# Kernel optimization log

Hardware: AMD Instinct MI355X
Metric: run time of the kernel (lower is better)

## Reference

```python
import jax, jax.numpy as jnp
import numpy as np

N_HEADS = 16
GROUP_SIZE = 4
D_MODEL = 2048
N_GROUPS = N_HEADS // GROUP_SIZE  # 4 KV heads
HEAD_DIM = D_MODEL // N_HEADS     # 128
B, S = 2, 2048


def setup_inputs() -> dict:
    key = jax.random.key(0)
    ks = jax.random.split(key, 10)
    sd = 1.0 / np.sqrt(D_MODEL)
    inp = {
        "x": jax.random.normal(ks[0], (B, S, D_MODEL), dtype=jnp.float32),
        # per-position, per-pair rotation angles (llama-style freqs)
        "rotary_freqs": jax.random.uniform(ks[1], (S, HEAD_DIM // 2), dtype=jnp.float32) * 6.283,
        # weights stored as [in, out] so forward is x @ W + b
        "Wq": jax.random.normal(ks[2], (D_MODEL, D_MODEL), dtype=jnp.float32) * sd,
        "bq": jnp.zeros((D_MODEL,), dtype=jnp.float32),
        "Wk": jax.random.normal(ks[3], (D_MODEL, N_GROUPS * HEAD_DIM), dtype=jnp.float32) * sd,
        "bk": jnp.zeros((N_GROUPS * HEAD_DIM,), dtype=jnp.float32),
        "Wv": jax.random.normal(ks[4], (D_MODEL, N_GROUPS * HEAD_DIM), dtype=jnp.float32) * sd,
        "bv": jnp.zeros((N_GROUPS * HEAD_DIM,), dtype=jnp.float32),
        "Wo": jax.random.normal(ks[5], (D_MODEL, D_MODEL), dtype=jnp.float32) * sd,
        "bo": jnp.zeros((D_MODEL,), dtype=jnp.float32),
    }
    return inp


def _rope(t, cos, sin):
    # t: [B, S, H, head_dim]; cos/sin: [1, S, 1, head_dim//2]
    t2 = t.reshape(t.shape[:-1] + (HEAD_DIM // 2, 2))
    te, to = t2[..., 0], t2[..., 1]
    re = te * cos - to * sin
    ro = te * sin + to * cos
    return jnp.stack([re, ro], axis=-1).reshape(t.shape)


def reference(x, rotary_freqs, Wq, bq, Wk, bk, Wv, bv, Wo, bo):
    Bx, Sx, _ = x.shape
    q = (x @ Wq + bq).reshape(Bx, Sx, N_HEADS, HEAD_DIM)
    k = (x @ Wk + bk).reshape(Bx, Sx, N_GROUPS, HEAD_DIM)
    v = (x @ Wv + bv).reshape(Bx, Sx, N_GROUPS, HEAD_DIM)

    cos = jnp.cos(rotary_freqs)[None, :, None, :]
    sin = jnp.sin(rotary_freqs)[None, :, None, :]
    q = _rope(q, cos, sin)
    k = _rope(k, cos, sin)

    q = q.transpose(0, 2, 1, 3)  # [B, H, S, hd]
    k = k.transpose(0, 2, 1, 3)  # [B, G, S, hd]
    v = v.transpose(0, 2, 1, 3)  # [B, G, S, hd]

    rep = N_HEADS // N_GROUPS
    k = jnp.repeat(k, rep, axis=1)  # repeat_interleave over head dim
    v = jnp.repeat(v, rep, axis=1)

    scores = jnp.einsum("bhsd,bhtd->bhst", q, k) / jnp.sqrt(jnp.float32(HEAD_DIM))
    att = jax.nn.softmax(scores, axis=-1)
    out = jnp.einsum("bhst,bhtd->bhsd", att, v)  # [B, H, S, hd]
    out = out.transpose(0, 2, 1, 3).reshape(Bx, Sx, D_MODEL)
    return out @ Wo + bo
```

## Files before the change

kernel.cpp:

```cpp
#include <hip/hip_runtime.h>
#include <cstdint>
#include <cstddef>

#define NB 2
#define SEQ 2048
#define DMODEL 2048
#define NHEAD 16
#define HDIM 128
#define NGRP 4
#define NKV (NGRP * HDIM)
#define NQKV (DMODEL + 2 * NKV)
#define MROWS (NB * SEQ)
#define QSCALE_LOG2E 0.12751743f

typedef unsigned short u16_t;
typedef unsigned int u32_t;
typedef __bf16 bf16x8 __attribute__((ext_vector_type(8)));
typedef __bf16 bf16x4 __attribute__((ext_vector_type(4)));
typedef float f32x4 __attribute__((ext_vector_type(4)));

static __device__ __forceinline__ u16_t f2bf(float f) {
  u32_t u = __builtin_bit_cast(u32_t, f);
  u32_t r = u + 0x7FFFu + ((u >> 16) & 1u);
  return (u16_t)(r >> 16);
}


__global__ __launch_bounds__(256) void k_prep(
    const float* __restrict__ x, const float* __restrict__ rf,
    const float* __restrict__ bq, const float* __restrict__ bk, const float* __restrict__ bv,
    const float* __restrict__ Wq, const float* __restrict__ Wk,
    const float* __restrict__ Wv, const float* __restrict__ Wo,
    u16_t* __restrict__ xb, float* __restrict__ cosT, float* __restrict__ sinT,
    float* __restrict__ bqkv, u16_t* __restrict__ Wqkvt, u16_t* __restrict__ Wot) {
  __shared__ float tile[64][65];
  int bid = blockIdx.x, t = threadIdx.x;

  if (bid < 8192) {
    int i = bid * 256 + t;
    float4 v = ((const float4*)x)[i];
    uint2 pk;
    pk.x = (u32_t)f2bf(v.x) | ((u32_t)f2bf(v.y) << 16);
    pk.y = (u32_t)f2bf(v.z) | ((u32_t)f2bf(v.w) << 16);
    ((uint2*)xb)[i] = pk;
    return;
  }
  bid -= 8192;
  if (bid < 512) {
    int i = bid * 256 + t;
    float f = rf[i];
    cosT[i] = cosf(f);
    sinT[i] = sinf(f);
    return;
  }
  bid -= 512;
  if (bid < 12) {
    int i = bid * 256 + t;
    float v = (i < DMODEL) ? bq[i] : (i < DMODEL + NKV ? bk[i - DMODEL] : bv[i - DMODEL - NKV]);
    bqkv[i] = v;
    return;
  }
  bid -= 12;

  const float* W; u16_t* Wt; int N, n0, k0;
  if (bid < 1024) {
    W = Wq; Wt = Wqkvt; N = DMODEL;
    n0 = (bid & 31) * 64; k0 = (bid >> 5) * 64;
  } else if (bid < 1280) {
    int b2 = bid - 1024;
    W = Wk; Wt = Wqkvt + (size_t)DMODEL * DMODEL; N = NKV;
    n0 = (b2 & 7) * 64; k0 = (b2 >> 3) * 64;
  } else if (bid < 1536) {
    int b2 = bid - 1280;
    W = Wv; Wt = Wqkvt + (size_t)(DMODEL + NKV) * DMODEL; N = NKV;
    n0 = (b2 & 7) * 64; k0 = (b2 >> 3) * 64;
  } else {
    int b2 = bid - 1536;
    W = Wo; Wt = Wot; N = DMODEL;
    n0 = (b2 & 31) * 64; k0 = (b2 >> 5) * 64;
  }
  const int K = DMODEL;
#pragma unroll
  for (int pass = 0; pass < 4; ++pass) {
    int slot = pass * 256 + t;
    int r = slot >> 4, c4 = (slot & 15) * 4;
    float4 v = *(const float4*)(W + (size_t)(k0 + r) * N + n0 + c4);
    tile[r][c4] = v.x; tile[r][c4 + 1] = v.y; tile[r][c4 + 2] = v.z; tile[r][c4 + 3] = v.w;
  }
  __syncthreads();
  int nr = t >> 2, seg = t & 3;
  alignas(16) u16_t o[16];
#pragma unroll
  for (int kk = 0; kk < 16; ++kk) o[kk] = f2bf(tile[seg * 16 + kk][nr]);
  u16_t* dst = Wt + (size_t)(n0 + nr) * K + k0 + seg * 16;
  ((int4*)dst)[0] = ((const int4*)o)[0];
  ((int4*)dst)[1] = ((const int4*)o)[1];
}


template <int EPI>
__global__ __launch_bounds__(512, 4) void k_gemm(
    const u16_t* __restrict__ A, const u16_t* __restrict__ Bt, const float* __restrict__ bias,
    float* __restrict__ Cout, u16_t* __restrict__ Qb, u16_t* __restrict__ Kb,
    u16_t* __restrict__ Vt, const float* __restrict__ cosT, const float* __restrict__ sinT,
    int M, int N, int K) {
  __shared__ u16_t lds[32768];
  int tid = threadIdx.x;
  int wid = tid >> 6, lane = tid & 63;
  int l15 = lane & 15, l4 = lane >> 4;
  int wrow = wid >> 2, wcol = wid & 3;

  int m0 = blockIdx.y << 7, n0 = blockIdx.x << 7;

  f32x4 acc[4][2] = {};

  auto stage = [&](int t) {
    u16_t* Al = lds + (t & 1) * 8192;
    u16_t* Bl = lds + 16384 + (t & 1) * 8192;
    int kbase = t * 64;
#pragma unroll
    for (int ss = 0; ss < 2; ++ss) {
      int slot = tid + ss * 512;
      int row = slot >> 3, c = slot & 7;
      int cs = c ^ (row & 7);
      __builtin_amdgcn_global_load_lds(
          (const __attribute__((address_space(1))) u32_t*)(A + (size_t)(m0 + row) * K + kbase + cs * 8),
          (__attribute__((address_space(3))) u32_t*)(Al + slot * 8), 16, 0, 0);
      __builtin_amdgcn_global_load_lds(
          (const __attribute__((address_space(1))) u32_t*)(Bt + (size_t)(n0 + row) * K + kbase + cs * 8),
          (__attribute__((address_space(3))) u32_t*)(Bl + slot * 8), 16, 0, 0);
    }
  };

  stage(0);
  stage(1);

  const int NT = K >> 6;
  for (int t = 0; t < NT; ++t) {
    if (t == NT - 1) {
      asm volatile("s_waitcnt vmcnt(0)" ::: "memory");
    } else {
      asm volatile("s_waitcnt vmcnt(4)" ::: "memory");
    }
    __builtin_amdgcn_s_barrier();
    __builtin_amdgcn_sched_barrier(0);

    const u16_t* Acur = lds + (t & 1) * 8192;
    const u16_t* Bcur = lds + 16384 + (t & 1) * 8192;

#pragma unroll
    for (int kk = 0; kk < 2; ++kk) {
      int chunk = ((kk << 2) + l4) ^ (l15 & 7);
      bf16x8 af[4], bfr[2];
#pragma unroll
      for (int i = 0; i < 4; ++i)
        af[i] = *(const bf16x8*)(Acur + (wrow * 64 + i * 16 + l15) * 64 + chunk * 8);
#pragma unroll
      for (int j = 0; j < 2; ++j)
        bfr[j] = *(const bf16x8*)(Bcur + (wcol * 32 + j * 16 + l15) * 64 + chunk * 8);

      __builtin_amdgcn_s_setprio(1);
#pragma unroll
      for (int i = 0; i < 4; ++i)
#pragma unroll
        for (int j = 0; j < 2; ++j)
          acc[i][j] = __builtin_amdgcn_mfma_f32_16x16x32_bf16(af[i], bfr[j], acc[i][j], 0, 0, 0);
      __builtin_amdgcn_s_setprio(0);
    }

    __builtin_amdgcn_sched_barrier(0);
    __builtin_amdgcn_s_barrier();
    __builtin_amdgcn_sched_barrier(0);
    if (t + 2 < NT) stage(t + 2);
  }

  if (EPI == 0) {
#pragma unroll
    for (int j = 0; j < 2; ++j) {
      int n = n0 + wcol * 32 + j * 16 + l15;
      float bs = bias[n];
#pragma unroll
      for (int i = 0; i < 4; ++i) {
        int mbase = m0 + wrow * 64 + i * 16 + l4 * 4;
#pragma unroll
        for (int r = 0; r < 4; ++r)
          Cout[(size_t)(mbase + r) * N + n] = acc[i][j][r] + bs;
      }
    }
  } else {
    bool isV = (n0 >= DMODEL + NKV);
    bool isK = (n0 >= DMODEL) && !isV;
#pragma unroll
    for (int j = 0; j < 2; ++j) {
      int n = n0 + wcol * 32 + j * 16 + l15;
      float bs = bias[n];
      int d = n & (HDIM - 1);
      int p = d >> 1;
      bool evn = !(d & 1);
#pragma unroll
      for (int i = 0; i < 4; ++i) {
        int mbase = m0 + wrow * 64 + i * 16 + l4 * 4;
        if (isV) {
          int g = (n - DMODEL - NKV) >> 7;
          int b = mbase >> 11, s0 = mbase & (SEQ - 1);
          u16_t o[4];
#pragma unroll
          for (int r = 0; r < 4; ++r) o[r] = f2bf(acc[i][j][r] + bs);
          uint2 pk;
          pk.x = (u32_t)o[0] | ((u32_t)o[1] << 16);
          pk.y = (u32_t)o[2] | ((u32_t)o[3] << 16);
          *(uint2*)(Vt + ((size_t)(b * NGRP + g) * HDIM + d) * SEQ + s0) = pk;
        } else {
#pragma unroll
          for (int r = 0; r < 4; ++r) {
            int m = mbase + r;
            int b = m >> 11, s = m & (SEQ - 1);
            float val = acc[i][j][r] + bs;
            float pv = __shfl_xor(val, 1);
            float c = cosT[s * (HDIM / 2) + p];
            float sn = sinT[s * (HDIM / 2) + p];
            float outv = evn ? (val * c - pv * sn) : (pv * sn + val * c);
            if (isK) {
              int g = (n - DMODEL) >> 7;
              Kb[((size_t)(b * NGRP + g) * SEQ + s) * HDIM + d] = f2bf(outv);
            } else {
              int h = n >> 7;
              Qb[((size_t)(b * NHEAD + h) * SEQ + s) * HDIM + d] = f2bf(outv * QSCALE_LOG2E);
            }
          }
        }
      }
    }
  }
}


__global__ __launch_bounds__(256, 2) void k_attn(
    const u16_t* __restrict__ Qb, const u16_t* __restrict__ Kb, const u16_t* __restrict__ Vt,
    u16_t* __restrict__ attn_out) {
  __shared__ u16_t lds[40960];

  int tid = threadIdx.x, wid = tid >> 6, lane = tid & 63;
  int l15 = lane & 15, l4 = lane >> 4;
  int bh = blockIdx.y;
  int b = bh >> 4, h = bh & 15, g = h >> 2;
  int q0 = blockIdx.x * 128;
  const u16_t* Qhead = Qb + (size_t)(b * NHEAD + h) * SEQ * HDIM;
  const u16_t* Khead = Kb + (size_t)(b * NGRP + g) * SEQ * HDIM;
  const u16_t* Vhead = Vt + (size_t)(b * NGRP + g) * HDIM * SEQ;

  bf16x8 qfa[4], qfb[4];
#pragma unroll
  for (int kc = 0; kc < 4; ++kc) {
    qfa[kc] = *(const bf16x8*)(Qhead + (size_t)(q0 + wid * 32 + l15) * HDIM + kc * 32 + l4 * 8);
    qfb[kc] = *(const bf16x8*)(Qhead + (size_t)(q0 + wid * 32 + 16 + l15) * HDIM + kc * 32 + l4 * 8);
  }

  f32x4 oa[8] = {}, ob[8] = {};
  f32x4 lav = {0.f, 0.f, 0.f, 0.f}, lbv = {0.f, 0.f, 0.f, 0.f};

  auto stageK = [&](int kv0, int ks) {
    u16_t* Kl = lds + ks * 8192;
#pragma unroll
    for (int ss = 0; ss < 4; ++ss) {
      int slot = tid + ss * 256;
      int rK = slot >> 4;
      int cK = (slot & 15) ^ ((rK & 3) | (((rK >> 3) & 1) << 2));
      __builtin_amdgcn_global_load_lds(
          (const __attribute__((address_space(1))) u32_t*)(Khead + (size_t)(kv0 + rK) * HDIM + cK * 8),
          (__attribute__((address_space(3))) u32_t*)(Kl + slot * 8), 16, 0, 0);
    }
  };
  auto stageV = [&](int kv0, int vs) {
    u16_t* Vl = lds + 24576 + vs * 8192;
#pragma unroll
    for (int ss = 0; ss < 4; ++ss) {
      int slot = tid + ss * 256;
      int rV = slot >> 3, cV = (slot & 7) ^ (rV & 7);
      __builtin_amdgcn_global_load_lds(
          (const __attribute__((address_space(1))) u32_t*)(Vhead + (size_t)rV * SEQ + kv0 + cV * 8),
          (__attribute__((address_space(3))) u32_t*)(Vl + slot * 8), 16, 0, 0);
    }
  };

  auto qk = [&](int ks, f32x4 (&Sa)[4], f32x4 (&Sb)[4]) {
    const u16_t* Kcur = lds + ks * 8192;
#pragma unroll
    for (int kc = 0; kc < 4; ++kc) {
#pragma unroll
      for (int kvb = 0; kvb < 4; ++kvb) {
        int row = (l15 >> 2) * 8 + ((kvb & 1) << 2) + (l15 & 3) + ((kvb >> 1) << 5);
        int chunk = ((kc << 2) + l4) ^ (l15 & 7);
        bf16x8 kf = *(const bf16x8*)(Kcur + row * 128 + chunk * 8);
        Sa[kvb] = __builtin_amdgcn_mfma_f32_16x16x32_bf16(kf, qfa[kc], Sa[kvb], 0, 0, 0);
        Sb[kvb] = __builtin_amdgcn_mfma_f32_16x16x32_bf16(kf, qfb[kc], Sb[kvb], 0, 0, 0);
      }
    }
  };

  auto expand = [&](f32x4 (&Sa)[4], f32x4 (&Sb)[4], bf16x8 (&pfa)[2], bf16x8 (&pfb)[2]) {
    bf16x4 pa[4], pb[4];
#pragma unroll
    for (int kvb = 0; kvb < 4; ++kvb) {
#pragma unroll
      for (int r = 0; r < 4; ++r) {
        float ea = __builtin_amdgcn_exp2f(Sa[kvb][r]);
        float eb = __builtin_amdgcn_exp2f(Sb[kvb][r]);
        lav[r] += ea; lbv[r] += eb;
        pa[kvb][r] = (__bf16)ea;
        pb[kvb][r] = (__bf16)eb;
      }
    }
#pragma unroll
    for (int kc2 = 0; kc2 < 2; ++kc2) {
      uint2 alo = __builtin_bit_cast(uint2, pa[kc2 * 2]);
      uint2 ahi = __builtin_bit_cast(uint2, pa[kc2 * 2 + 1]);
      uint4 wa; wa.x = alo.x; wa.y = alo.y; wa.z = ahi.x; wa.w = ahi.y;
      pfa[kc2] = __builtin_bit_cast(bf16x8, wa);
      uint2 blo = __builtin_bit_cast(uint2, pb[kc2 * 2]);
      uint2 bhi = __builtin_bit_cast(uint2, pb[kc2 * 2 + 1]);
      uint4 wb; wb.x = blo.x; wb.y = blo.y; wb.z = bhi.x; wb.w = bhi.y;
      pfb[kc2] = __builtin_bit_cast(bf16x8, wb);
    }
  };

  auto pv = [&](int vs, bf16x8 (&pfa)[2], bf16x8 (&pfb)[2]) {
    const u16_t* Vcur = lds + 24576 + vs * 8192;
#pragma unroll
    for (int kc2 = 0; kc2 < 2; ++kc2) {
#pragma unroll
      for (int dcb = 0; dcb < 8; ++dcb) {
        int chunk = ((kc2 << 2) + l4) ^ (l15 & 7);
        bf16x8 vf = *(const bf16x8*)(Vcur + (dcb * 16 + l15) * 64 + chunk * 8);
        oa[dcb] = __builtin_amdgcn_mfma_f32_16x16x32_bf16(vf, pfa[kc2], oa[dcb], 0, 0, 0);
        ob[dcb] = __builtin_amdgcn_mfma_f32_16x16x32_bf16(vf, pfb[kc2], ob[dcb], 0, 0, 0);
      }
    }
  };

  const int NT = SEQ / 64;

  auto step = [&](int t, bool last, f32x4 (&Ia)[4], f32x4 (&Ib)[4],
                  f32x4 (&Oa)[4], f32x4 (&Ob)[4]) {
    bf16x8 pfa[2], pfb[2];
    expand(Ia, Ib, pfa, pfb);
    if (last) {
      asm volatile("s_waitcnt vmcnt(4)" ::: "memory");
    } else {
      asm volatile("s_waitcnt vmcnt(8)" ::: "memory");
    }
    __builtin_amdgcn_s_barrier();
    __builtin_amdgcn_sched_barrier(0);
#pragma unroll
    for (int z = 0; z < 4; ++z)
#pragma unroll
      for (int r = 0; r < 4; ++r) { Oa[z][r] = 0.f; Ob[z][r] = 0.f; }
    __builtin_amdgcn_s_setprio(1);
    pv(t & 1, pfa, pfb);
    qk((t + 1) % 3, Oa, Ob);
    __builtin_amdgcn_s_setprio(0);
    __builtin_amdgcn_sched_barrier(0);
    __builtin_amdgcn_s_barrier();
    __builtin_amdgcn_sched_barrier(0);
    if (t + 3 < NT) stageK((t + 3) * 64, t % 3);
    if (t + 2 < NT) stageV((t + 2) * 64, t & 1);
  };

  f32x4 sA[4] = {}, sB[4] = {}, tA[4], tB[4];

  stageK(0, 0);
  stageK(64, 1);
  stageV(0, 0);
  asm volatile("s_waitcnt vmcnt(8)" ::: "memory");
  __builtin_amdgcn_s_barrier();
  __builtin_amdgcn_sched_barrier(0);
  stageK(128, 2);
  stageV(64, 1);
  qk(0, sA, sB);

  for (int p = 0; p < 15; ++p) {
    step(2 * p, false, sA, sB, tA, tB);
    step(2 * p + 1, false, tA, tB, sA, sB);
  }
  step(30, true, sA, sB, tA, tB);
  {
    bf16x8 pfa[2], pfb[2];
    expand(tA, tB, pfa, pfb);
    asm volatile("s_waitcnt vmcnt(0)" ::: "memory");
    __builtin_amdgcn_s_barrier();
    __builtin_amdgcn_sched_barrier(0);
    pv(1, pfa, pfb);
  }

  float la = lav[0] + lav[1] + lav[2] + lav[3];
  float lb = lbv[0] + lbv[1] + lbv[2] + lbv[3];
  la += __shfl_xor(la, 16); la += __shfl_xor(la, 32);
  lb += __shfl_xor(lb, 16); lb += __shfl_xor(lb, 32);
  float inva = 1.0f / la, invb = 1.0f / lb;

#pragma unroll
  for (int half = 0; half < 2; ++half) {
    u16_t* Owave = lds + half * 8704 + wid * 2176;
    const f32x4* oacc = half ? ob : oa;
    float inv = half ? invb : inva;
#pragma unroll
    for (int dcb = 0; dcb < 8; ++dcb) {
      bf16x4 ov;
#pragma unroll
      for (int r = 0; r < 4; ++r) ov[r] = (__bf16)(oacc[dcb][r] * inv);
      *(uint2*)(Owave + l15 * 136 + dcb * 16 + l4 * 4) = __builtin_bit_cast(uint2, ov);
    }
#pragma unroll
    for (int pass = 0; pass < 4; ++pass) {
      int rowq = pass * 4 + l4;
      int4 v = *(const int4*)(Owave + rowq * 136 + l15 * 8);
      int s = q0 + wid * 32 + half * 16 + rowq;
      *(int4*)(attn_out + ((size_t)(b * SEQ + s)) * DMODEL + h * HDIM + l15 * 8) = v;
    }
  }
}


extern "C" void kernel_launch(void* const* d_in, const int* in_sizes, int n_in,
                              void* d_out, int out_size, void* d_ws, size_t ws_size,
                              hipStream_t stream) {
  (void)in_sizes; (void)n_in; (void)out_size; (void)ws_size;
  const float* x  = (const float*)d_in[0];
  const float* rf = (const float*)d_in[1];
  const float* Wq = (const float*)d_in[2];
  const float* bq = (const float*)d_in[3];
  const float* Wk = (const float*)d_in[4];
  const float* bk = (const float*)d_in[5];
  const float* Wv = (const float*)d_in[6];
  const float* bv = (const float*)d_in[7];
  const float* Wo = (const float*)d_in[8];
  const float* bo = (const float*)d_in[9];
  float* out = (float*)d_out;

  char* ws = (char*)d_ws;
  u16_t* xb    = (u16_t*)ws;  ws += (size_t)MROWS * DMODEL * 2;
  u16_t* Wqkvt = (u16_t*)ws;  ws += (size_t)NQKV * DMODEL * 2;
  u16_t* Wot   = (u16_t*)ws;  ws += (size_t)DMODEL * DMODEL * 2;
  float* bqkv  = (float*)ws;  ws += (size_t)NQKV * 4;
  float* cosT  = (float*)ws;  ws += (size_t)SEQ * (HDIM / 2) * 4;
  float* sinT  = (float*)ws;  ws += (size_t)SEQ * (HDIM / 2) * 4;
  u16_t* Qb    = (u16_t*)ws;  ws += (size_t)NB * NHEAD * SEQ * HDIM * 2;
  u16_t* Kb    = (u16_t*)ws;  ws += (size_t)NB * NGRP * SEQ * HDIM * 2;
  u16_t* Vt    = (u16_t*)ws;  ws += (size_t)NB * NGRP * HDIM * SEQ * 2;
  u16_t* attn  = xb;

  k_prep<<<11276, 256, 0, stream>>>(x, rf, bq, bk, bv, Wq, Wk, Wv, Wo,
                                    xb, cosT, sinT, bqkv, Wqkvt, Wot);

  k_gemm<1><<<dim3(NQKV / 128, MROWS / 128), 512, 0, stream>>>(
      xb, Wqkvt, bqkv, nullptr, Qb, Kb, Vt, cosT, sinT, MROWS, NQKV, DMODEL);

  dim3 ga(SEQ / 128, NB * NHEAD);
  k_attn<<<ga, 256, 0, stream>>>(Qb, Kb, Vt, attn);

  k_gemm<0><<<dim3(DMODEL / 128, MROWS / 128), 512, 0, stream>>>(
      attn, Wot, bo, out, nullptr, nullptr, nullptr, nullptr, nullptr, MROWS, DMODEL, DMODEL);
}
```

Measured before the change: 177.3 us.

## Double-buffer K and V together in attention and shrink LDS footprint

Replaces the triple-buffered K plus double-buffered V staging with one combined double-buffered K/V stage, cutting shared memory from 80 KB to 64 KB per block. Each step now waits for all outstanding loads (vmcnt(0)) instead of leaving the next tile in flight, which simplifies the pipeline and removes the special-case last step. The softmax row-sum accumulator also collapses from a 4-wide vector to a scalar. The shallower prefetch exposes more global-load latency, and the scalar sum adds a serial dependency chain in the exp loop.

```diff
diff --git a/kernel.cpp b/kernel.cpp
--- a/kernel.cpp
+++ b/kernel.cpp
@@ -238,7 +238,7 @@
 __global__ __launch_bounds__(256, 2) void k_attn(
     const u16_t* __restrict__ Qb, const u16_t* __restrict__ Kb, const u16_t* __restrict__ Vt,
     u16_t* __restrict__ attn_out) {
-  __shared__ u16_t lds[40960];
+  __shared__ u16_t lds[32768];
 
   int tid = threadIdx.x, wid = tid >> 6, lane = tid & 63;
   int l15 = lane & 15, l4 = lane >> 4;
@@ -257,10 +257,11 @@
   }
 
   f32x4 oa[8] = {}, ob[8] = {};
-  f32x4 lav = {0.f, 0.f, 0.f, 0.f}, lbv = {0.f, 0.f, 0.f, 0.f};
-
-  auto stageK = [&](int kv0, int ks) {
-    u16_t* Kl = lds + ks * 8192;
+  float la = 0.f, lb = 0.f;
+
+  auto stage = [&](int kv0, int bufIdx) {
+    u16_t* Kl = lds + bufIdx * 8192;
+    u16_t* Vl = lds + 16384 + bufIdx * 8192;
 #pragma unroll
     for (int ss = 0; ss < 4; ++ss) {
       int slot = tid + ss * 256;
@@ -269,13 +270,6 @@
       __builtin_amdgcn_global_load_lds(
           (const __attribute__((address_space(1))) u32_t*)(Khead + (size_t)(kv0 + rK) * HDIM + cK * 8),
           (__attribute__((address_space(3))) u32_t*)(Kl + slot * 8), 16, 0, 0);
-    }
-  };
-  auto stageV = [&](int kv0, int vs) {
-    u16_t* Vl = lds + 24576 + vs * 8192;
-#pragma unroll
-    for (int ss = 0; ss < 4; ++ss) {
-      int slot = tid + ss * 256;
       int rV = slot >> 3, cV = (slot & 7) ^ (rV & 7);
       __builtin_amdgcn_global_load_lds(
           (const __attribute__((address_space(1))) u32_t*)(Vhead + (size_t)rV * SEQ + kv0 + cV * 8),
@@ -283,8 +277,8 @@
     }
   };
 
-  auto qk = [&](int ks, f32x4 (&Sa)[4], f32x4 (&Sb)[4]) {
-    const u16_t* Kcur = lds + ks * 8192;
+  auto qk = [&](int bufIdx, f32x4 (&Sa)[4], f32x4 (&Sb)[4]) {
+    const u16_t* Kcur = lds + bufIdx * 8192;
 #pragma unroll
     for (int kc = 0; kc < 4; ++kc) {
 #pragma unroll
@@ -306,7 +300,7 @@
       for (int r = 0; r < 4; ++r) {
         float ea = __builtin_amdgcn_exp2f(Sa[kvb][r]);
         float eb = __builtin_amdgcn_exp2f(Sb[kvb][r]);
-        lav[r] += ea; lbv[r] += eb;
+        la += ea; lb += eb;
         pa[kvb][r] = (__bf16)ea;
         pb[kvb][r] = (__bf16)eb;
       }
@@ -324,8 +318,8 @@
     }
   };
 
-  auto pv = [&](int vs, bf16x8 (&pfa)[2], bf16x8 (&pfb)[2]) {
-    const u16_t* Vcur = lds + 24576 + vs * 8192;
+  auto pv = [&](int bufIdx, bf16x8 (&pfa)[2], bf16x8 (&pfb)[2]) {
+    const u16_t* Vcur = lds + 16384 + bufIdx * 8192;
 #pragma unroll
     for (int kc2 = 0; kc2 < 2; ++kc2) {
 #pragma unroll
@@ -338,17 +332,10 @@
     }
   };
 
-  const int NT = SEQ / 64;
-
-  auto step = [&](int t, bool last, f32x4 (&Ia)[4], f32x4 (&Ib)[4],
-                  f32x4 (&Oa)[4], f32x4 (&Ob)[4]) {
+  auto step = [&](int t, f32x4 (&Ia)[4], f32x4 (&Ib)[4], f32x4 (&Oa)[4], f32x4 (&Ob)[4]) {
     bf16x8 pfa[2], pfb[2];
     expand(Ia, Ib, pfa, pfb);
-    if (last) {
-      asm volatile("s_waitcnt vmcnt(4)" ::: "memory");
-    } else {
-      asm volatile("s_waitcnt vmcnt(8)" ::: "memory");
-    }
+    asm volatile("s_waitcnt vmcnt(0)" ::: "memory");
     __builtin_amdgcn_s_barrier();
     __builtin_amdgcn_sched_barrier(0);
 #pragma unroll
@@ -357,43 +344,34 @@
       for (int r = 0; r < 4; ++r) { Oa[z][r] = 0.f; Ob[z][r] = 0.f; }
     __builtin_amdgcn_s_setprio(1);
     pv(t & 1, pfa, pfb);
-    qk((t + 1) % 3, Oa, Ob);
+    qk((t + 1) & 1, Oa, Ob);
     __builtin_amdgcn_s_setprio(0);
     __builtin_amdgcn_sched_barrier(0);
     __builtin_amdgcn_s_barrier();
     __builtin_amdgcn_sched_barrier(0);
-    if (t + 3 < NT) stageK((t + 3) * 64, t % 3);
-    if (t + 2 < NT) stageV((t + 2) * 64, t & 1);
+    if (t + 2 < SEQ / 64) stage((t + 2) * 64, t & 1);
   };
 
   f32x4 sA[4] = {}, sB[4] = {}, tA[4], tB[4];
 
-  stageK(0, 0);
-  stageK(64, 1);
-  stageV(0, 0);
+  stage(0, 0);
+  stage(64, 1);
   asm volatile("s_waitcnt vmcnt(8)" ::: "memory");
   __builtin_amdgcn_s_barrier();
   __builtin_amdgcn_sched_barrier(0);
-  stageK(128, 2);
-  stageV(64, 1);
   qk(0, sA, sB);
 
   for (int p = 0; p < 15; ++p) {
-    step(2 * p, false, sA, sB, tA, tB);
-    step(2 * p + 1, false, tA, tB, sA, sB);
-  }
-  step(30, true, sA, sB, tA, tB);
+    step(2 * p, sA, sB, tA, tB);
+    step(2 * p + 1, tA, tB, sA, sB);
+  }
+  step(30, sA, sB, tA, tB);
   {
     bf16x8 pfa[2], pfb[2];
     expand(tA, tB, pfa, pfb);
-    asm volatile("s_waitcnt vmcnt(0)" ::: "memory");
-    __builtin_amdgcn_s_barrier();
-    __builtin_amdgcn_sched_barrier(0);
     pv(1, pfa, pfb);
   }
 
-  float la = lav[0] + lav[1] + lav[2] + lav[3];
-  float lb = lbv[0] + lbv[1] + lbv[2] + lbv[3];
   la += __shfl_xor(la, 16); la += __shfl_xor(la, 32);
   lb += __shfl_xor(lb, 16); lb += __shfl_xor(lb, 32);
   float inva = 1.0f / la, invb = 1.0f / lb;
```

New measurement: 174.5 us (median of 2 runs). About the same (-1.6%).
